# Kernel tuning notes

Hardware: AMD Instinct MI355X
Metric: run time of the kernel (lower is better)

Reference implementation:

```python
import jax, jax.numpy as jnp
import numpy as np
import math

EMBED_DIM = 512
NUM_HEADS = 8
HEAD_DIM = EMBED_DIM // NUM_HEADS


def setup_inputs() -> dict:
    key = jax.random.key(0)
    ks = jax.random.split(key, 11)
    s = 1.0 / math.sqrt(EMBED_DIM)
    x = jax.random.normal(ks[0], (8, EMBED_DIM, 32, 32), dtype=jnp.float32)
    Wq = jax.random.uniform(ks[1], (EMBED_DIM, EMBED_DIM), jnp.float32, -s, s)
    bq = jax.random.uniform(ks[2], (EMBED_DIM,), jnp.float32, -s, s)
    Wk = jax.random.uniform(ks[3], (EMBED_DIM, EMBED_DIM), jnp.float32, -s, s)
    bk = jax.random.uniform(ks[4], (EMBED_DIM,), jnp.float32, -s, s)
    Wv = jax.random.uniform(ks[5], (EMBED_DIM, EMBED_DIM), jnp.float32, -s, s)
    bv = jax.random.uniform(ks[6], (EMBED_DIM,), jnp.float32, -s, s)
    Wo = jax.random.uniform(ks[7], (EMBED_DIM, EMBED_DIM), jnp.float32, -s, s)
    bo = jax.random.uniform(ks[8], (EMBED_DIM,), jnp.float32, -s, s)
    gamma = jnp.ones((EMBED_DIM,), jnp.float32)
    beta = jnp.zeros((EMBED_DIM,), jnp.float32)
    return {"x": x, "Wq": Wq, "bq": bq, "Wk": Wk, "bk": bk, "Wv": Wv,
            "bv": bv, "Wo": Wo, "bo": bo, "gamma": gamma, "beta": beta}


def layer_norm(x, gamma, beta, eps=1e-5):
    mu = jnp.mean(x, axis=-1, keepdims=True)
    var = jnp.mean(jnp.square(x - mu), axis=-1, keepdims=True)
    return (x - mu) * jax.lax.rsqrt(var + eps) * gamma + beta


def reference(x, Wq, bq, Wk, bk, Wv, bv, Wo, bo, gamma, beta):
    B, C, H, W = x.shape
    S = H * W
    # [B, S, C]
    x_flat = x.reshape(B, C, S).transpose(0, 2, 1)
    residual = x_flat
    xn = layer_norm(x_flat, gamma, beta)
    # torch Linear: y = x @ W^T + b
    q = (xn @ Wq.T + bq).reshape(B, S, NUM_HEADS, HEAD_DIM)
    k = (xn @ Wk.T + bk).reshape(B, S, NUM_HEADS, HEAD_DIM)
    v = (xn @ Wv.T + bv).reshape(B, S, NUM_HEADS, HEAD_DIM)
    scale = 1.0 / math.sqrt(HEAD_DIM)
    scores = jnp.einsum('bqhd,bkhd->bhqk', q, k) * scale
    attn = jax.nn.softmax(scores, axis=-1)  # dropout is identity in eval
    out = jnp.einsum('bhqk,bkhd->bqhd', attn, v).reshape(B, S, C)
    out = out @ Wo.T + bo + residual
    return out.transpose(0, 2, 1).reshape(B, C, H, W)
```

## Files before the change

kernel.cpp:

```cpp
#include <hip/hip_runtime.h>
#include <hip/hip_bf16.h>

typedef __bf16 bf16_t;
typedef __bf16 bf16x8 __attribute__((ext_vector_type(8)));
typedef float floatx4 __attribute__((ext_vector_type(4)));

#define EMBED 512
#define S_LEN 1024
#define NH 8
#define HD 64
#define LDK 1056
#define LDV 1088

#define MFMA16(a, b, c) __builtin_amdgcn_mfma_f32_16x16x32_bf16(a, b, c, 0, 0, 0)

static __device__ __forceinline__ bf16_t f2bf(float f) {
    unsigned int x = __builtin_bit_cast(unsigned int, f);
    unsigned int lsb = (x >> 16) & 1u;
    x += 0x7fffu + lsb;
    unsigned short u = (unsigned short)(x >> 16);
    return __builtin_bit_cast(bf16_t, u);
}
static __device__ __forceinline__ float bf2f(bf16_t v) {
    unsigned short u = __builtin_bit_cast(unsigned short, v);
    unsigned int x = ((unsigned int)u) << 16;
    return __builtin_bit_cast(float, x);
}
static __device__ __forceinline__ unsigned int pack2(float lo, float hi) {
    return (__builtin_bit_cast(unsigned int, lo) >> 16) |
           (__builtin_bit_cast(unsigned int, hi) & 0xFFFF0000u);
}
static __device__ __forceinline__ unsigned int pack2r(float lo, float hi) {
    unsigned short a = __builtin_bit_cast(unsigned short, f2bf(lo));
    unsigned short b = __builtin_bit_cast(unsigned short, f2bf(hi));
    return (unsigned int)a | ((unsigned int)b << 16);
}

__global__ __launch_bounds__(256) void cvt4_kernel(const float* __restrict__ s0,
                                                   const float* __restrict__ s1,
                                                   const float* __restrict__ s2,
                                                   const float* __restrict__ s3,
                                                   bf16_t* __restrict__ d0,
                                                   bf16_t* __restrict__ d1,
                                                   bf16_t* __restrict__ d2,
                                                   bf16_t* __restrict__ d3) {
    const float* s; bf16_t* d;
    switch (blockIdx.y) {
        case 0:  s = s0; d = d0; break;
        case 1:  s = s1; d = d1; break;
        case 2:  s = s2; d = d2; break;
        default: s = s3; d = d3; break;
    }
    int i = (blockIdx.x * 256 + threadIdx.x) * 8;
#pragma unroll
    for (int j = 0; j < 8; ++j) d[i + j] = f2bf(s[i + j]);
}

__global__ __launch_bounds__(256) void ln_stats_kernel(const float* __restrict__ x,
                                                       float* __restrict__ muA,
                                                       float* __restrict__ rsA) {
    int bid = blockIdx.x;
    int b = bid >> 5, s0 = (bid & 31) * 32;
    int t = threadIdx.x, tc = t >> 5, ts = t & 31;
    const float* xp = x + (size_t)b * EMBED * S_LEN + s0 + ts;
    float sm = 0.f, sq = 0.f;
    for (int i = 0; i < 64; ++i) {
        float v = xp[(size_t)(tc * 64 + i) * S_LEN];
        sm += v; sq += v * v;
    }
    __shared__ float Sm[8][32], Sq[8][32];
    Sm[tc][ts] = sm; Sq[tc][ts] = sq;
    __syncthreads();
    if (t < 32) {
        float m = 0.f, q = 0.f;
#pragma unroll
        for (int j = 0; j < 8; ++j) { m += Sm[j][t]; q += Sq[j][t]; }
        float mu = m * (1.0f / EMBED);
        float var = q * (1.0f / EMBED) - mu * mu;
        muA[b * S_LEN + s0 + t] = mu;
        rsA[b * S_LEN + s0 + t] = rsqrtf(var + 1e-5f);
    }
}

__global__ __launch_bounds__(256) void ln_tr_kernel(const float* __restrict__ x,
                                                    const float* __restrict__ muA,
                                                    const float* __restrict__ rsA,
                                                    const float* __restrict__ gamma,
                                                    const float* __restrict__ beta,
                                                    bf16_t* __restrict__ xn) {
    __shared__ float T[32][33];
    int tx = threadIdx.x & 31, ty = threadIdx.x >> 5;
    int b = blockIdx.z, c0 = blockIdx.y * 32, s0 = blockIdx.x * 32;
#pragma unroll
    for (int i = 0; i < 4; ++i) {
        int cr = ty + i * 8;
        T[cr][tx] = x[((size_t)b * EMBED + c0 + cr) * S_LEN + s0 + tx];
    }
    __syncthreads();
    float g = gamma[c0 + tx], be = beta[c0 + tx];
#pragma unroll
    for (int i = 0; i < 4; ++i) {
        int sr = ty + i * 8;
        float mu = muA[b * S_LEN + s0 + sr];
        float rs = rsA[b * S_LEN + s0 + sr];
        xn[((size_t)b * S_LEN + s0 + sr) * EMBED + c0 + tx] =
            f2bf((T[tx][sr] - mu) * rs * g + be);
    }
}

__global__ __launch_bounds__(256) void gemm_kernel(const bf16_t* __restrict__ X,
                                                   const bf16_t* __restrict__ W,
                                                   const float* __restrict__ b0,
                                                   const float* __restrict__ b1,
                                                   const float* __restrict__ b2,
                                                   bf16_t* __restrict__ Y,
                                                   bf16_t* __restrict__ vtb) {
    __shared__ __align__(16) bf16_t Wl[2][128 * 72];
    int t = threadIdx.x;
    int col0 = blockIdx.y * 128, row0 = blockIdx.x * 128;
    int scol = t >> 1, sseg = (t & 1) * 32;
    const bf16_t* wsrc = W + (size_t)(col0 + scol) * EMBED + sseg;
    {
        bf16x8 r0 = *(const bf16x8*)(wsrc);
        bf16x8 r1 = *(const bf16x8*)(wsrc + 8);
        bf16x8 r2 = *(const bf16x8*)(wsrc + 16);
        bf16x8 r3 = *(const bf16x8*)(wsrc + 24);
        bf16_t* d = &Wl[0][scol * 72 + sseg];
        *(bf16x8*)d = r0;        *(bf16x8*)(d + 8) = r1;
        *(bf16x8*)(d + 16) = r2; *(bf16x8*)(d + 24) = r3;
    }
    int lane = t & 63, w = t >> 6, g = lane >> 4, n16 = lane & 15;
    int rw0 = row0 + w * 32;
    const bf16_t* xr0 = X + (size_t)(rw0 + n16) * EMBED + g * 8;
    const bf16_t* xr1 = xr0 + (size_t)16 * EMBED;
    bf16x8 a00 = *(const bf16x8*)(xr0);
    bf16x8 a01 = *(const bf16x8*)(xr0 + 32);
    bf16x8 a10 = *(const bf16x8*)(xr1);
    bf16x8 a11 = *(const bf16x8*)(xr1 + 32);
    __syncthreads();
    floatx4 acc[2][8] = {};
#pragma unroll
    for (int kc = 0; kc < 8; ++kc) {
        bf16x8 p0, p1, p2, p3, na00, na01, na10, na11;
        if (kc < 7) {
            int ko = (kc + 1) * 64;
            p0 = *(const bf16x8*)(wsrc + ko);
            p1 = *(const bf16x8*)(wsrc + ko + 8);
            p2 = *(const bf16x8*)(wsrc + ko + 16);
            p3 = *(const bf16x8*)(wsrc + ko + 24);
            na00 = *(const bf16x8*)(xr0 + ko);
            na01 = *(const bf16x8*)(xr0 + ko + 32);
            na10 = *(const bf16x8*)(xr1 + ko);
            na11 = *(const bf16x8*)(xr1 + ko + 32);
        }
        const bf16_t* wl = &Wl[kc & 1][0];
#pragma unroll
        for (int kk = 0; kk < 2; ++kk) {
            bf16x8 s0 = (kk == 0) ? a00 : a01;
            bf16x8 s1 = (kk == 0) ? a10 : a11;
#pragma unroll
            for (int nt = 0; nt < 8; ++nt) {
                bf16x8 bfr = *(const bf16x8*)(&wl[(nt * 16 + n16) * 72 + kk * 32 + g * 8]);
                acc[0][nt] = MFMA16(s0, bfr, acc[0][nt]);
                acc[1][nt] = MFMA16(s1, bfr, acc[1][nt]);
            }
        }
        if (kc < 7) {
            bf16_t* d = &Wl[(kc + 1) & 1][scol * 72 + sseg];
            *(bf16x8*)d = p0;        *(bf16x8*)(d + 8) = p1;
            *(bf16x8*)(d + 16) = p2; *(bf16x8*)(d + 24) = p3;
            a00 = na00; a01 = na01; a10 = na10; a11 = na11;
        }
        __syncthreads();
    }
    if (col0 < 1024) {
        const float* bp = (col0 < 512) ? b0 : b1;
#pragma unroll
        for (int ar = 0; ar < 2; ++ar)
#pragma unroll
            for (int nt = 0; nt < 8; ++nt) {
                int col = col0 + nt * 16 + n16;
                float bv = bp[col & 511];
#pragma unroll
                for (int r = 0; r < 4; ++r) {
                    int row = rw0 + ar * 16 + g * 4 + r;
                    Y[(size_t)row * LDK + col] = f2bf(acc[ar][nt][r] + bv);
                }
            }
    } else {
        bf16_t* Tl = &Wl[0][0];
#pragma unroll
        for (int ar = 0; ar < 2; ++ar)
#pragma unroll
            for (int nt = 0; nt < 8; ++nt) {
                int chl = nt * 16 + n16;
                float bv = b2[(col0 & 511) + chl];
                uint2 pr;
                pr.x = pack2r(acc[ar][nt][0] + bv, acc[ar][nt][1] + bv);
                pr.y = pack2r(acc[ar][nt][2] + bv, acc[ar][nt][3] + bv);
                *(uint2*)(&Tl[chl * 136 + w * 32 + ar * 16 + g * 4]) = pr;
            }
        __syncthreads();
        int ch = t >> 1, seg = (t & 1) * 64;
        int bb = row0 >> 10, s0 = row0 & 1023;
        bf16_t* dst = vtb + ((size_t)(bb * EMBED + (col0 - 1024) + ch)) * LDV + s0 + seg;
        const bf16_t* srcl = &Tl[ch * 136 + seg];
#pragma unroll
        for (int i = 0; i < 8; ++i)
            *(bf16x8*)(dst + i * 8) = *(const bf16x8*)(srcl + i * 8);
    }
}

__global__ __launch_bounds__(256) void wsgemm_out_kernel(const bf16_t* __restrict__ Wb,
                                                         const bf16_t* __restrict__ act,
                                                         const float* __restrict__ bias,
                                                         const float* __restrict__ xres,
                                                         float* __restrict__ out) {
    __shared__ __align__(16) bf16_t Al[2][64 * 72];
    int b = blockIdx.z, n0 = blockIdx.x * 64, m0 = blockIdx.y * 128;
    int t = threadIdx.x;
    int srow = t >> 2, sseg = (t & 3) * 16;
    const bf16_t* asrc = act + ((size_t)b * S_LEN + n0 + srow) * EMBED + sseg;
    {
        bf16x8 r0 = *(const bf16x8*)(asrc);
        bf16x8 r1 = *(const bf16x8*)(asrc + 8);
        bf16_t* d = &Al[0][srow * 72 + sseg];
        *(bf16x8*)d = r0; *(bf16x8*)(d + 8) = r1;
    }
    int lane = t & 63, w = t >> 6, g = lane >> 4, n16 = lane & 15;
    int mw = m0 + w * 32;
    const bf16_t* wr0 = Wb + (size_t)(mw + n16) * EMBED + g * 8;
    const bf16_t* wr1 = wr0 + (size_t)16 * EMBED;
    bf16x8 a00 = *(const bf16x8*)(wr0);
    bf16x8 a01 = *(const bf16x8*)(wr0 + 32);
    bf16x8 a10 = *(const bf16x8*)(wr1);
    bf16x8 a11 = *(const bf16x8*)(wr1 + 32);
    __syncthreads();
    floatx4 acc[2][4] = {};
#pragma unroll
    for (int kc = 0; kc < 8; ++kc) {
        bf16x8 p0, p1, na00, na01, na10, na11;
        if (kc < 7) {
            int ko = (kc + 1) * 64;
            p0 = *(const bf16x8*)(asrc + ko);
            p1 = *(const bf16x8*)(asrc + ko + 8);
            na00 = *(const bf16x8*)(wr0 + ko);
            na01 = *(const bf16x8*)(wr0 + ko + 32);
            na10 = *(const bf16x8*)(wr1 + ko);
            na11 = *(const bf16x8*)(wr1 + ko + 32);
        }
        const bf16_t* al = &Al[kc & 1][0];
#pragma unroll
        for (int kk = 0; kk < 2; ++kk) {
            bf16x8 s0 = (kk == 0) ? a00 : a01;
            bf16x8 s1 = (kk == 0) ? a10 : a11;
#pragma unroll
            for (int nt = 0; nt < 4; ++nt) {
                bf16x8 bfr = *(const bf16x8*)(&al[(nt * 16 + n16) * 72 + kk * 32 + g * 8]);
                acc[0][nt] = MFMA16(s0, bfr, acc[0][nt]);
                acc[1][nt] = MFMA16(s1, bfr, acc[1][nt]);
            }
        }
        if (kc < 7) {
            bf16_t* d = &Al[(kc + 1) & 1][srow * 72 + sseg];
            *(bf16x8*)d = p0; *(bf16x8*)(d + 8) = p1;
            a00 = na00; a01 = na01; a10 = na10; a11 = na11;
        }
        __syncthreads();
    }
#pragma unroll
    for (int ar = 0; ar < 2; ++ar)
#pragma unroll
        for (int r = 0; r < 4; ++r) {
            int row = mw + ar * 16 + g * 4 + r;
            float bv = bias[row];
#pragma unroll
            for (int nt = 0; nt < 4; ++nt) {
                int col = n0 + nt * 16 + n16;
                size_t oi = ((size_t)b * EMBED + row) * S_LEN + col;
                out[oi] = acc[ar][nt][r] + bv + xres[oi];
            }
        }
}

__global__ __launch_bounds__(256) void attn_kernel(const bf16_t* __restrict__ qk,
                                                   const bf16_t* __restrict__ vt,
                                                   bf16_t* __restrict__ o) {
    __shared__ __align__(16) bf16_t Kt[2][64 * 72];
    __shared__ __align__(16) bf16_t Vl2[2][64 * 72];
    __shared__ __align__(16) unsigned int Pl[4][2][16 * 36];
    int bid = blockIdx.x;
    int bh = bid & 63, qt = bid >> 6;
    int b = bh >> 3, h = bh & 7;
    int t = threadIdx.x, w = t >> 6, lane = t & 63, g = lane >> 4, n16 = lane & 15;
    size_t baseQK = (size_t)b * S_LEN * LDK;
    size_t baseV  = ((size_t)b * EMBED + h * HD) * LDV;
    int qA = qt * 128 + w * 32 + n16;

    const bf16_t* qpA = qk + baseQK + (size_t)qA * LDK + h * HD + g * 8;
    const bf16_t* qpB = qpA + (size_t)16 * LDK;
    bf16x8 qa0 = *(const bf16x8*)(qpA);
    bf16x8 qa1 = *(const bf16x8*)(qpA + 32);
    bf16x8 qb0 = *(const bf16x8*)(qpB);
    bf16x8 qb1 = *(const bf16x8*)(qpB + 32);
#pragma unroll
    for (int j = 0; j < 8; ++j) {
        qa0[j] = f2bf(bf2f(qa0[j]) * 0.125f);
        qa1[j] = f2bf(bf2f(qa1[j]) * 0.125f);
        qb0[j] = f2bf(bf2f(qb0[j]) * 0.125f);
        qb1[j] = f2bf(bf2f(qb1[j]) * 0.125f);
    }
    const bf16_t* kbase = qk + baseQK + 512 + h * HD;
    const bf16_t* vbase = vt + baseV;

    int srow = t >> 2, scol = (t & 3) * 16;
    const bf16_t* ksrc = kbase + (size_t)srow * LDK + scol;
    const bf16_t* vsrc = vbase + (size_t)srow * LDV + scol;
    {
        bf16x8 k0 = *(const bf16x8*)(ksrc);
        bf16x8 k1 = *(const bf16x8*)(ksrc + 8);
        bf16x8 v0 = *(const bf16x8*)(vsrc);
        bf16x8 v1 = *(const bf16x8*)(vsrc + 8);
        bf16_t* kd = &Kt[0][srow * 72 + scol];
        bf16_t* vd = &Vl2[0][srow * 72 + scol];
        *(bf16x8*)kd = k0; *(bf16x8*)(kd + 8) = k1;
        *(bf16x8*)vd = v0; *(bf16x8*)(vd + 8) = v1;
    }

    float lsA[4] = {}, lsB[4] = {};
    floatx4 oaccA[4] = {}, oaccB[4] = {};
    unsigned int* PLa = &Pl[w][0][0];
    unsigned int* PLb = &Pl[w][1][0];

    for (int it = 0; it < 16; ++it) {
        int cur = it & 1, nxt = cur ^ 1;
        __syncthreads();
        bf16x8 pk0, pk1, pv0, pv1;
        if (it < 15) {
            const bf16_t* kp = ksrc + (size_t)(it + 1) * 64 * LDK;
            pk0 = *(const bf16x8*)(kp);
            pk1 = *(const bf16x8*)(kp + 8);
            const bf16_t* vp = vsrc + (it + 1) * 64;
            pv0 = *(const bf16x8*)(vp);
            pv1 = *(const bf16x8*)(vp + 8);
        }
        const bf16_t* Kl = &Kt[cur][0];
        const bf16_t* Vl = &Vl2[cur][0];
        floatx4 sA[4], sB[4];
#pragma unroll
        for (int kb = 0; kb < 4; ++kb) {
            bf16x8 k0 = *(const bf16x8*)(&Kl[(kb * 16 + n16) * 72 + g * 8]);
            bf16x8 k1 = *(const bf16x8*)(&Kl[(kb * 16 + n16) * 72 + 32 + g * 8]);
            sA[kb] = floatx4{-12.f, -12.f, -12.f, -12.f};
            sA[kb] = MFMA16(k0, qa0, sA[kb]);
            sA[kb] = MFMA16(k1, qa1, sA[kb]);
            sB[kb] = floatx4{-12.f, -12.f, -12.f, -12.f};
            sB[kb] = MFMA16(k0, qb0, sB[kb]);
            sB[kb] = MFMA16(k1, qb1, sB[kb]);
        }
        if (it < 15) {
            bf16_t* kd = &Kt[nxt][srow * 72 + scol];
            bf16_t* vd = &Vl2[nxt][srow * 72 + scol];
            *(bf16x8*)kd = pk0; *(bf16x8*)(kd + 8) = pk1;
            *(bf16x8*)vd = pv0; *(bf16x8*)(vd + 8) = pv1;
        }
#pragma unroll
        for (int kb = 0; kb < 4; ++kb)
#pragma unroll
            for (int r = 0; r < 4; ++r) {
                float eA = __expf(fminf(sA[kb][r], 40.f));
                sA[kb][r] = eA; lsA[kb] += eA;
                float eB = __expf(fminf(sB[kb][r], 40.f));
                sB[kb][r] = eB; lsB[kb] += eB;
            }
#pragma unroll
        for (int kb = 0; kb < 4; ++kb) {
            uint2 prA, prB;
            prA.x = pack2(sA[kb][0], sA[kb][1]);
            prA.y = pack2(sA[kb][2], sA[kb][3]);
            *(uint2*)&PLa[n16 * 36 + kb * 8 + g * 2] = prA;
            prB.x = pack2(sB[kb][0], sB[kb][1]);
            prB.y = pack2(sB[kb][2], sB[kb][3]);
            *(uint2*)&PLb[n16 * 36 + kb * 8 + g * 2] = prB;
        }
        uint4 uA0 = *(const uint4*)&PLa[n16 * 36 + g * 4];
        uint4 uA1 = *(const uint4*)&PLa[n16 * 36 + 16 + g * 4];
        uint4 uB0 = *(const uint4*)&PLb[n16 * 36 + g * 4];
        uint4 uB1 = *(const uint4*)&PLb[n16 * 36 + 16 + g * 4];
        bf16x8 pfA0 = __builtin_bit_cast(bf16x8, uA0);
        bf16x8 pfA1 = __builtin_bit_cast(bf16x8, uA1);
        bf16x8 pfB0 = __builtin_bit_cast(bf16x8, uB0);
        bf16x8 pfB1 = __builtin_bit_cast(bf16x8, uB1);
#pragma unroll
        for (int dt = 0; dt < 4; ++dt) {
            bf16x8 v0 = *(const bf16x8*)(&Vl[(dt * 16 + n16) * 72 + g * 8]);
            bf16x8 v1 = *(const bf16x8*)(&Vl[(dt * 16 + n16) * 72 + 32 + g * 8]);
            oaccA[dt] = MFMA16(v0, pfA0, oaccA[dt]);
            oaccA[dt] = MFMA16(v1, pfA1, oaccA[dt]);
            oaccB[dt] = MFMA16(v0, pfB0, oaccB[dt]);
            oaccB[dt] = MFMA16(v1, pfB1, oaccB[dt]);
        }
    }
    float lA = (lsA[0] + lsA[1]) + (lsA[2] + lsA[3]);
    lA += __shfl_xor(lA, 16);
    lA += __shfl_xor(lA, 32);
    float lB = (lsB[0] + lsB[1]) + (lsB[2] + lsB[3]);
    lB += __shfl_xor(lB, 16);
    lB += __shfl_xor(lB, 32);
    float rlA = 1.0f / lA, rlB = 1.0f / lB;
    size_t orowA = ((size_t)b * S_LEN + qA) * EMBED + h * HD;
    size_t orowB = orowA + (size_t)16 * EMBED;
#pragma unroll
    for (int dt = 0; dt < 4; ++dt) {
        uint2 prA, prB;
        prA.x = pack2(oaccA[dt][0] * rlA, oaccA[dt][1] * rlA);
        prA.y = pack2(oaccA[dt][2] * rlA, oaccA[dt][3] * rlA);
        *(uint2*)(o + orowA + dt * 16 + g * 4) = prA;
        prB.x = pack2(oaccB[dt][0] * rlB, oaccB[dt][1] * rlB);
        prB.y = pack2(oaccB[dt][2] * rlB, oaccB[dt][3] * rlB);
        *(uint2*)(o + orowB + dt * 16 + g * 4) = prB;
    }
}

extern "C" void kernel_launch(void* const* d_in, const int* in_sizes, int n_in,
                              void* d_out, int out_size, void* d_ws, size_t ws_size,
                              hipStream_t stream) {
    const float* x     = (const float*)d_in[0];
    const float* Wq    = (const float*)d_in[1];
    const float* bq    = (const float*)d_in[2];
    const float* Wk    = (const float*)d_in[3];
    const float* bk    = (const float*)d_in[4];
    const float* Wv    = (const float*)d_in[5];
    const float* bv    = (const float*)d_in[6];
    const float* Wo    = (const float*)d_in[7];
    const float* bo    = (const float*)d_in[8];
    const float* gamma = (const float*)d_in[9];
    const float* beta  = (const float*)d_in[10];
    float* out = (float*)d_out;

    char* ws = (char*)d_ws;
    bf16_t* xn    = (bf16_t*)ws;
    bf16_t* qkb   = (bf16_t*)(ws + 8388608);
    bf16_t* wqkv  = (bf16_t*)(ws + 25690112);
    bf16_t* wo    = (bf16_t*)(ws + 27262976);
    float*  muA   = (float*)(ws + 27787264);
    float*  rsA   = (float*)(ws + 27820032);
    bf16_t* ab    = xn;

    bf16_t* vtb = (bf16_t*)d_out;

    cvt4_kernel<<<dim3(128, 4), 256, 0, stream>>>(Wq, Wk, Wv, Wo,
                                                  wqkv, wqkv + 262144,
                                                  wqkv + 524288, wo);
    ln_stats_kernel<<<dim3(256), 256, 0, stream>>>(x, muA, rsA);
    ln_tr_kernel<<<dim3(32, 16, 8), 256, 0, stream>>>(x, muA, rsA, gamma, beta, xn);
    gemm_kernel<<<dim3(64, 12), 256, 0, stream>>>(xn, wqkv, bq, bk, bv, qkb, vtb);
    attn_kernel<<<dim3(512), 256, 0, stream>>>(qkb, vtb, ab);
    wsgemm_out_kernel<<<dim3(16, 4, 8), 256, 0, stream>>>(wo, ab, bo, x, out);
}
```

Measured before the change: 171.1 us.

## Fuse layernorm stats and transpose into one kernel; share P scratch in attention

Merges the separate layernorm statistics and normalize-transpose kernels into one kernel. Each block loads a 32-position by 512-channel slab of x into a swizzled LDS tile, computes mean and rstd there, and writes normalized bf16 rows with vectorized stores. This removes one kernel launch and the second full read of x, at the cost of about 67KB of LDS per block, which limits occupancy. The attention kernel also halves its per-wave P staging buffer by writing and reading the A and B halves one after the other, which lowers LDS use but serializes those two stages.

```diff
diff --git a/kernel.cpp b/kernel.cpp
--- a/kernel.cpp
+++ b/kernel.cpp
@@ -56,55 +56,70 @@
     for (int j = 0; j < 8; ++j) d[i + j] = f2bf(s[i + j]);
 }
 
-__global__ __launch_bounds__(256) void ln_stats_kernel(const float* __restrict__ x,
-                                                       float* __restrict__ muA,
-                                                       float* __restrict__ rsA) {
+__global__ __launch_bounds__(256) void ln_fused_kernel(const float* __restrict__ x,
+                                                       const float* __restrict__ gamma,
+                                                       const float* __restrict__ beta,
+                                                       bf16_t* __restrict__ xn) {
+    __shared__ float T[32][521];
+    __shared__ float Pm[32][33], Pq[32][33];
+    __shared__ float Mu[32], Rs[32];
     int bid = blockIdx.x;
     int b = bid >> 5, s0 = (bid & 31) * 32;
-    int t = threadIdx.x, tc = t >> 5, ts = t & 31;
-    const float* xp = x + (size_t)b * EMBED * S_LEN + s0 + ts;
-    float sm = 0.f, sq = 0.f;
-    for (int i = 0; i < 64; ++i) {
-        float v = xp[(size_t)(tc * 64 + i) * S_LEN];
-        sm += v; sq += v * v;
-    }
-    __shared__ float Sm[8][32], Sq[8][32];
-    Sm[tc][ts] = sm; Sq[tc][ts] = sq;
+    int t = threadIdx.x;
+    int lc = t >> 3;
+    int si = (t & 7) * 4;
+    const float* xp = x + ((size_t)b * EMBED + lc) * S_LEN + s0 + si;
+    float sm[4] = {}, sq[4] = {};
+#pragma unroll
+    for (int p = 0; p < 16; ++p) {
+        int c = lc + p * 32;
+        float4 v = *(const float4*)(xp + (size_t)p * 32 * S_LEN);
+        int cs = c ^ ((c >> 3) & 0x38);
+        T[si + 0][cs] = v.x; T[si + 1][cs] = v.y;
+        T[si + 2][cs] = v.z; T[si + 3][cs] = v.w;
+        sm[0] += v.x; sq[0] += v.x * v.x;
+        sm[1] += v.y; sq[1] += v.y * v.y;
+        sm[2] += v.z; sq[2] += v.z * v.z;
+        sm[3] += v.w; sq[3] += v.w * v.w;
+    }
+#pragma unroll
+    for (int k = 0; k < 4; ++k) { Pm[si + k][lc] = sm[k]; Pq[si + k][lc] = sq[k]; }
     __syncthreads();
     if (t < 32) {
         float m = 0.f, q = 0.f;
 #pragma unroll
-        for (int j = 0; j < 8; ++j) { m += Sm[j][t]; q += Sq[j][t]; }
+        for (int j = 0; j < 32; ++j) { m += Pm[t][j]; q += Pq[t][j]; }
         float mu = m * (1.0f / EMBED);
         float var = q * (1.0f / EMBED) - mu * mu;
-        muA[b * S_LEN + s0 + t] = mu;
-        rsA[b * S_LEN + s0 + t] = rsqrtf(var + 1e-5f);
-    }
-}
-
-__global__ __launch_bounds__(256) void ln_tr_kernel(const float* __restrict__ x,
-                                                    const float* __restrict__ muA,
-                                                    const float* __restrict__ rsA,
-                                                    const float* __restrict__ gamma,
-                                                    const float* __restrict__ beta,
-                                                    bf16_t* __restrict__ xn) {
-    __shared__ float T[32][33];
-    int tx = threadIdx.x & 31, ty = threadIdx.x >> 5;
-    int b = blockIdx.z, c0 = blockIdx.y * 32, s0 = blockIdx.x * 32;
-#pragma unroll
-    for (int i = 0; i < 4; ++i) {
-        int cr = ty + i * 8;
-        T[cr][tx] = x[((size_t)b * EMBED + c0 + cr) * S_LEN + s0 + tx];
+        Mu[t] = mu; Rs[t] = rsqrtf(var + 1e-5f);
     }
     __syncthreads();
-    float g = gamma[c0 + tx], be = beta[c0 + tx];
-#pragma unroll
-    for (int i = 0; i < 4; ++i) {
-        int sr = ty + i * 8;
-        float mu = muA[b * S_LEN + s0 + sr];
-        float rs = rsA[b * S_LEN + s0 + sr];
-        xn[((size_t)b * S_LEN + s0 + sr) * EMBED + c0 + tx] =
-            f2bf((T[tx][sr] - mu) * rs * g + be);
+    int cidx = t & 31;
+    int rw = t >> 5;
+#pragma unroll
+    for (int rg = 0; rg < 4; ++rg) {
+        int srl = rg * 8 + rw;
+        float mu = Mu[srl], rs = Rs[srl];
+        int cb = cidx * 16;
+        bf16_t* dst = xn + ((size_t)b * S_LEN + s0 + srl) * EMBED + cb;
+#pragma unroll
+        for (int h = 0; h < 2; ++h) {
+            int c0h = cb + h * 8;
+            float4 g0 = *(const float4*)(gamma + c0h);
+            float4 g1 = *(const float4*)(gamma + c0h + 4);
+            float4 be0 = *(const float4*)(beta + c0h);
+            float4 be1 = *(const float4*)(beta + c0h + 4);
+            float gv[8] = {g0.x, g0.y, g0.z, g0.w, g1.x, g1.y, g1.z, g1.w};
+            float bv[8] = {be0.x, be0.y, be0.z, be0.w, be1.x, be1.y, be1.z, be1.w};
+            bf16x8 o;
+#pragma unroll
+            for (int j = 0; j < 8; ++j) {
+                int c = c0h + j;
+                int cs = c ^ ((c >> 3) & 0x38);
+                o[j] = f2bf((T[srl][cs] - mu) * rs * gv[j] + bv[j]);
+            }
+            *(bf16x8*)(dst + h * 8) = o;
+        }
     }
 }
 
@@ -288,7 +303,7 @@
                                                    bf16_t* __restrict__ o) {
     __shared__ __align__(16) bf16_t Kt[2][64 * 72];
     __shared__ __align__(16) bf16_t Vl2[2][64 * 72];
-    __shared__ __align__(16) unsigned int Pl[4][2][16 * 36];
+    __shared__ __align__(16) unsigned int Pl[4][16 * 36];
     int bid = blockIdx.x;
     int bh = bid & 63, qt = bid >> 6;
     int b = bh >> 3, h = bh & 7;
@@ -329,8 +344,7 @@
 
     float lsA[4] = {}, lsB[4] = {};
     floatx4 oaccA[4] = {}, oaccB[4] = {};
-    unsigned int* PLa = &Pl[w][0][0];
-    unsigned int* PLb = &Pl[w][1][0];
+    unsigned int* PLw = &Pl[w][0];
 
     for (int it = 0; it < 16; ++it) {
         int cur = it & 1, nxt = cur ^ 1;
@@ -375,20 +389,24 @@
             }
 #pragma unroll
         for (int kb = 0; kb < 4; ++kb) {
-            uint2 prA, prB;
-            prA.x = pack2(sA[kb][0], sA[kb][1]);
-            prA.y = pack2(sA[kb][2], sA[kb][3]);
-            *(uint2*)&PLa[n16 * 36 + kb * 8 + g * 2] = prA;
-            prB.x = pack2(sB[kb][0], sB[kb][1]);
-            prB.y = pack2(sB[kb][2], sB[kb][3]);
-            *(uint2*)&PLb[n16 * 36 + kb * 8 + g * 2] = prB;
-        }
-        uint4 uA0 = *(const uint4*)&PLa[n16 * 36 + g * 4];
-        uint4 uA1 = *(const uint4*)&PLa[n16 * 36 + 16 + g * 4];
-        uint4 uB0 = *(const uint4*)&PLb[n16 * 36 + g * 4];
-        uint4 uB1 = *(const uint4*)&PLb[n16 * 36 + 16 + g * 4];
+            uint2 pr;
+            pr.x = pack2(sA[kb][0], sA[kb][1]);
+            pr.y = pack2(sA[kb][2], sA[kb][3]);
+            *(uint2*)&PLw[n16 * 36 + kb * 8 + g * 2] = pr;
+        }
+        uint4 uA0 = *(const uint4*)&PLw[n16 * 36 + g * 4];
+        uint4 uA1 = *(const uint4*)&PLw[n16 * 36 + 16 + g * 4];
         bf16x8 pfA0 = __builtin_bit_cast(bf16x8, uA0);
         bf16x8 pfA1 = __builtin_bit_cast(bf16x8, uA1);
+#pragma unroll
+        for (int kb = 0; kb < 4; ++kb) {
+            uint2 pr;
+            pr.x = pack2(sB[kb][0], sB[kb][1]);
+            pr.y = pack2(sB[kb][2], sB[kb][3]);
+            *(uint2*)&PLw[n16 * 36 + kb * 8 + g * 2] = pr;
+        }
+        uint4 uB0 = *(const uint4*)&PLw[n16 * 36 + g * 4];
+        uint4 uB1 = *(const uint4*)&PLw[n16 * 36 + 16 + g * 4];
         bf16x8 pfB0 = __builtin_bit_cast(bf16x8, uB0);
         bf16x8 pfB1 = __builtin_bit_cast(bf16x8, uB1);
 #pragma unroll
@@ -443,8 +461,6 @@
     bf16_t* qkb   = (bf16_t*)(ws + 8388608);
     bf16_t* wqkv  = (bf16_t*)(ws + 25690112);
     bf16_t* wo    = (bf16_t*)(ws + 27262976);
-    float*  muA   = (float*)(ws + 27787264);
-    float*  rsA   = (float*)(ws + 27820032);
     bf16_t* ab    = xn;
 
     bf16_t* vtb = (bf16_t*)d_out;
@@ -452,8 +468,7 @@
     cvt4_kernel<<<dim3(128, 4), 256, 0, stream>>>(Wq, Wk, Wv, Wo,
                                                   wqkv, wqkv + 262144,
                                                   wqkv + 524288, wo);
-    ln_stats_kernel<<<dim3(256), 256, 0, stream>>>(x, muA, rsA);
-    ln_tr_kernel<<<dim3(32, 16, 8), 256, 0, stream>>>(x, muA, rsA, gamma, beta, xn);
+    ln_fused_kernel<<<dim3(256), 256, 0, stream>>>(x, gamma, beta, xn);
     gemm_kernel<<<dim3(64, 12), 256, 0, stream>>>(xn, wqkv, bq, bk, bv, qkb, vtb);
     attn_kernel<<<dim3(512), 256, 0, stream>>>(qkb, vtb, ab);
     wsgemm_out_kernel<<<dim3(16, 4, 8), 256, 0, stream>>>(wo, ab, bo, x, out);
```

Measured after the change: 169.1 us. Within noise of the previous version (-1.2%).
